# Kernel tuning notes

Measured on AMD Instinct MI355X. Metric: run time of the kernel, lower is better.

## Reference

```python
import jax, jax.numpy as jnp
import numpy as np

B, N, D = 8, 2048, 128
NEG = -9.0e15


def setup_inputs() -> dict:
    key = jax.random.key(0)
    ks = jax.random.split(key, 7)
    x = jax.random.normal(ks[0], (B, N, D), dtype=jnp.float32)
    # sparse-ish binary adjacency with self loops, stored dense as float
    adj = (jax.random.uniform(ks[1], (B, N, N)) < 0.1).astype(jnp.float32)
    adj = jnp.maximum(adj, jnp.eye(N, dtype=jnp.float32)[None])
    s = 1.0 / np.sqrt(D)
    W_w = jax.random.uniform(ks[2], (D, D), minval=-s, maxval=s, dtype=jnp.float32)
    W_b = jax.random.uniform(ks[3], (D,), minval=-s, maxval=s, dtype=jnp.float32)
    A = jnp.zeros((D, D), dtype=jnp.float32) + 0.01 * jax.random.normal(ks[4], (D, D), dtype=jnp.float32)
    s2 = 1.0 / np.sqrt(2 * D)
    gate_w = jax.random.uniform(ks[5], (1, 2 * D), minval=-s2, maxval=s2, dtype=jnp.float32)
    gate_b = jax.random.uniform(ks[6], (1,), minval=-s2, maxval=s2, dtype=jnp.float32)
    return {"x": x, "adj": adj, "W_w": W_w, "W_b": W_b, "A": A,
            "gate_w": gate_w, "gate_b": gate_b}


def reference(x, adj, W_w, W_b, A, gate_w, gate_b):
    # h = W(x): [B,N,D]
    h = jnp.einsum('bnf,df->bnd', x, W_w) + W_b
    # e[b,j,k] = (h A)[b,j,:] . h[b,k,:], then symmetrize
    hA = jnp.einsum('bnd,de->bne', h, A)
    e = jnp.einsum('bjl,bkl->bjk', hA, h)
    e = e + jnp.swapaxes(e, 1, 2)
    att = jnp.where(adj > 0, e, jnp.full_like(e, NEG))
    # NOTE: torch code softmaxes over dim=1 (the j axis)
    att = jax.nn.softmax(att, axis=1)
    att = att * adj
    h_prime = jax.nn.relu(jnp.einsum('bij,bjk->bik', att, h))
    gate_in = jnp.concatenate([x, h_prime], axis=-1)  # [B,N,2D]
    coeff = jax.nn.sigmoid(jnp.einsum('bnc,oc->bno', gate_in, gate_w) + gate_b)  # [B,N,1]
    return coeff * x + (1.0 - coeff) * h_prime
```

## Files before the change

### kernel.cpp

```cpp
#include <hip/hip_runtime.h>


#define B_ 8
#define N_ 2048
#define D_ 128

typedef __attribute__((ext_vector_type(8))) short short8;
typedef __attribute__((ext_vector_type(4))) float f32x4;

#define GLL(gp, lp) __builtin_amdgcn_global_load_lds( \
    (__attribute__((address_space(1))) const unsigned int*)(gp), \
    (__attribute__((address_space(3))) unsigned int*)(lp), 16, 0, 0)

static __device__ __forceinline__ unsigned short f2bf(float f) {
  union { float f; unsigned int u; } v; v.f = f;
  unsigned int r = v.u + 0x7fffu + ((v.u >> 16) & 1u);
  return (unsigned short)(r >> 16);
}
static __device__ __forceinline__ float bf2f(unsigned short u) {
  union { unsigned int u; float f; } v; v.u = ((unsigned int)u) << 16;
  return v.f;
}

#define CAT_OFF  ((size_t)0)
#define VT_OFF   ((size_t)8388608)
#define PUN_OFF  ((size_t)12582912)
#define S_OFF    ((size_t)79691776)
#define WB_OFF   ((size_t)79757312)
#define AT_OFF   ((size_t)79790080)
#define BITS_OFF ((size_t)79822848)

__global__ void k_cvt(const float* __restrict__ W, const float* __restrict__ A,
                      unsigned short* __restrict__ Wb1, unsigned short* __restrict__ Abt) {
  int t = threadIdx.x;
  for (int i = t; i < 128 * 128; i += 256) {
    Wb1[i] = f2bf(W[i]);
    Abt[(i & 127) * 128 + (i >> 7)] = f2bf(A[i]);
  }
}

__global__ __launch_bounds__(256) void k_bits2(const float* __restrict__ adj,
                                               unsigned int* __restrict__ bits) {
  size_t tid = (size_t)blockIdx.x * 256 + threadIdx.x;
  const float* p = adj + tid * 32;
  unsigned int m = 0;
#pragma unroll
  for (int i = 0; i < 8; i++) {
    f32x4 v = *(const f32x4*)(p + i * 4);
    m |= (v[0] > 0.f ? 1u : 0u) << (i * 4 + 0);
    m |= (v[1] > 0.f ? 1u : 0u) << (i * 4 + 1);
    m |= (v[2] > 0.f ? 1u : 0u) << (i * 4 + 2);
    m |= (v[3] > 0.f ? 1u : 0u) << (i * 4 + 3);
  }
  bits[tid] = m;
}

__global__ __launch_bounds__(256) void k1(const float* __restrict__ x,
                                          const unsigned short* __restrict__ Wb1,
                                          const float* __restrict__ Wbias,
                                          const unsigned short* __restrict__ Abt,
                                          unsigned short* __restrict__ cat) {
  __shared__ unsigned short hsm[4][16][136];
  __shared__ unsigned short hasm[4][16][136];
  const int t = threadIdx.x, w = t >> 6, lane = t & 63;
  const int q = lane >> 4, l15 = lane & 15;
  const size_t r0 = (size_t)blockIdx.x * 64 + w * 16;

  f32x4 acc[8];
#pragma unroll
  for (int dg = 0; dg < 8; dg++) acc[dg] = (f32x4){0.f, 0.f, 0.f, 0.f};
#pragma unroll
  for (int k = 0; k < 4; k++) {
    const float* xp = x + (r0 + l15) * 128 + k * 32 + q * 8;
    f32x4 xa = *(const f32x4*)xp;
    f32x4 xb = *(const f32x4*)(xp + 4);
    short8 af;
#pragma unroll
    for (int e = 0; e < 4; e++) { af[e] = (short)f2bf(xa[e]); af[4 + e] = (short)f2bf(xb[e]); }
#pragma unroll
    for (int dg = 0; dg < 8; dg++) {
      short8 bf = *(const short8*)(Wb1 + (dg * 16 + l15) * 128 + k * 32 + q * 8);
      acc[dg] = __builtin_amdgcn_mfma_f32_16x16x32_bf16(af, bf, acc[dg], 0, 0, 0);
    }
  }
#pragma unroll
  for (int dg = 0; dg < 8; dg++) {
    float bias = Wbias[dg * 16 + l15];
#pragma unroll
    for (int r = 0; r < 4; r++)
      hsm[w][q * 4 + r][dg * 16 + l15] = f2bf(acc[dg][r] + bias);
  }
  __syncthreads();
  f32x4 acc2[8];
#pragma unroll
  for (int dg = 0; dg < 8; dg++) acc2[dg] = (f32x4){0.f, 0.f, 0.f, 0.f};
#pragma unroll
  for (int k = 0; k < 4; k++) {
    short8 af = *(short8*)&hsm[w][l15][k * 32 + q * 8];
#pragma unroll
    for (int dg = 0; dg < 8; dg++) {
      short8 bf = *(const short8*)(Abt + (dg * 16 + l15) * 128 + k * 32 + q * 8);
      acc2[dg] = __builtin_amdgcn_mfma_f32_16x16x32_bf16(af, bf, acc2[dg], 0, 0, 0);
    }
  }
#pragma unroll
  for (int dg = 0; dg < 8; dg++)
#pragma unroll
    for (int r = 0; r < 4; r++)
      hasm[w][q * 4 + r][dg * 16 + l15] = f2bf(acc2[dg][r]);
  __syncthreads();
#pragma unroll
  for (int it = 0; it < 8; it++) {
    int idx = it * 64 + lane;
    int row = idx >> 5, c = idx & 31;
    short8 v = (c < 16) ? *(short8*)&hasm[w][row][c * 8]
                        : *(short8*)&hsm[w][row][(c - 16) * 8];
    *(short8*)(cat + ((r0 + row) << 8) + c * 8) = v;
  }
}

__global__ __launch_bounds__(256, 3) void k2(const unsigned short* __restrict__ cat,
                                             const unsigned int* __restrict__ bits,
                                             unsigned short* __restrict__ pun,
                                             float* __restrict__ s_out) {
  __shared__ unsigned short cj[64 * 256];
  const int t = threadIdx.x, w = t >> 6, lane = t & 63;
  const int q = lane >> 4, l15 = lane & 15;
  const int b = blockIdx.z;
  const int kbase = blockIdx.x * 128;
  const int j0b = blockIdx.y * 128;
  const size_t bN = (size_t)b * N_;
  const unsigned short* catp = cat + (bN << 8);
  const int kc = kbase + w * 32;
  const int kw = kc >> 5;
  short8 brg[2][8];
#pragma unroll
  for (int p = 0; p < 2; p++) {
    int krow = kc + 2 * l15 + p;
#pragma unroll
    for (int m = 0; m < 8; m++)
      brg[p][m] = *(const short8*)(catp + (((size_t)krow) << 8) +
                                   ((((m * 4 + q) + 16) & 31) * 8));
  }
  float acc0 = 0.f, acc1 = 0.f;
  for (int jt = 0; jt < 2; jt++) {
    const int j0 = j0b + jt * 64;
#pragma unroll
    for (int it = 0; it < 8; it++) {
      int sI = it * 256 + t;
      int row = sI >> 5, c = sI & 31;
      GLL(catp + (((size_t)(j0 + row)) << 8) + (c ^ (row & 7)) * 8,
          (char*)cj + sI * 16);
    }
    __syncthreads();
#pragma unroll
    for (int jsub = 0; jsub < 4; jsub++) {
      const int row = jsub * 16 + l15;
      short8 afr[8];
#pragma unroll
      for (int m = 0; m < 8; m++)
        afr[m] = *(short8*)(cj + row * 256 + (((m * 4 + q) ^ (l15 & 7)) * 8));
      f32x4 e0 = {0.f, 0.f, 0.f, 0.f}, e1 = {0.f, 0.f, 0.f, 0.f};
#pragma unroll
      for (int m = 0; m < 8; m++) {
        e0 = __builtin_amdgcn_mfma_f32_16x16x32_bf16(afr[m], brg[0][m], e0, 0, 0, 0);
        e1 = __builtin_amdgcn_mfma_f32_16x16x32_bf16(afr[m], brg[1][m], e1, 0, 0, 0);
      }
#pragma unroll
      for (int r = 0; r < 4; r++) {
        int jrow = j0 + jsub * 16 + q * 4 + r;
        unsigned int mb = bits[(bN + jrow) * 64 + kw];
        float x0 = ((mb >> (2 * l15)) & 1u) ? __expf(fminf(e0[r], 60.f)) : 0.f;
        float x1 = ((mb >> (2 * l15 + 1)) & 1u) ? __expf(fminf(e1[r], 60.f)) : 0.f;
        acc0 += x0; acc1 += x1;
        unsigned int pk = (unsigned int)f2bf(x0) | ((unsigned int)f2bf(x1) << 16);
        *(unsigned int*)(pun + ((bN + jrow) << 11) + kc + 2 * l15) = pk;
      }
    }
    __syncthreads();
  }
  acc0 += __shfl_xor(acc0, 16, 64); acc0 += __shfl_xor(acc0, 32, 64);
  acc1 += __shfl_xor(acc1, 16, 64); acc1 += __shfl_xor(acc1, 32, 64);
  if (lane < 16) {
    atomicAdd(&s_out[bN + kc + 2 * lane], acc0);
    atomicAdd(&s_out[bN + kc + 2 * lane + 1], acc1);
  }
}

__global__ __launch_bounds__(256) void k1v(const unsigned short* __restrict__ cat,
                                           const float* __restrict__ s,
                                           unsigned short* __restrict__ vt) {
  __shared__ unsigned short tile[64][136];
  __shared__ float rsv[64];
  const int t = threadIdx.x;
  const int b = blockIdx.y;
  const int nbase = blockIdx.x * 64;
  if (t < 64) rsv[t] = 1.f / s[(size_t)b * N_ + nbase + t];
#pragma unroll
  for (int k = 0; k < 4; k++) {
    int sI = t + 256 * k;
    int row = sI >> 4, part = sI & 15;
    *(short8*)&tile[row][part * 8] =
        *(const short8*)(cat + (((size_t)(b * N_ + nbase + row)) << 8) + 128 + part * 8);
  }
  __syncthreads();
#pragma unroll
  for (int k = 0; k < 4; k++) {
    int sI = t + 256 * k;
    int dd = sI >> 3, part = sI & 7;
    unsigned short tmp[8];
#pragma unroll
    for (int j = 0; j < 8; j++) {
      int jj = part * 8 + j;
      tmp[j] = f2bf(bf2f(tile[jj][dd]) * rsv[jj]);
    }
    *(short8*)(vt + (((size_t)(b * 128 + dd)) << 11) + nbase + part * 8) = *(short8*)tmp;
  }
}

__global__ __launch_bounds__(256) void k3(const unsigned short* __restrict__ pun,
                                          const unsigned short* __restrict__ vt,
                                          const float* __restrict__ x,
                                          const float* __restrict__ gw,
                                          const float* __restrict__ gb,
                                          float* __restrict__ out) {
  __shared__ char smem[40960];
  const int t = threadIdx.x, w = t >> 6, lane = t & 63;
  const int q = lane >> 4, l15 = lane & 15;
  const int b = blockIdx.y, i0 = blockIdx.x * 32;
  const size_t bN = (size_t)b * N_;
  unsigned short* pa = (unsigned short*)smem;
  unsigned short* vb = (unsigned short*)(smem + 8192);

  f32x4 acc[2][2];
#pragma unroll
  for (int ih = 0; ih < 2; ih++)
#pragma unroll
    for (int dh = 0; dh < 2; dh++) acc[ih][dh] = (f32x4){0.f, 0.f, 0.f, 0.f};

  for (int jt = 0; jt < N_ / 128; jt++) {
    const int j0 = jt * 128;
#pragma unroll
    for (int it = 0; it < 10; it++) {
      int sI = it * 256 + t;
      const unsigned short* g;
      if (sI < 512) {
        int row = sI >> 4, c = sI & 15;
        g = pun + (((size_t)(bN + i0 + row)) << 11) + j0 + ((c ^ (row & 7)) * 8);
      } else {
        int s2 = sI - 512;
        int dd = s2 >> 4, c = s2 & 15;
        g = vt + (((size_t)(b * 128 + dd)) << 11) + j0 + ((c ^ (dd & 7)) * 8);
      }
      GLL(g, smem + sI * 16);
    }
    __syncthreads();
#pragma unroll
    for (int ks = 0; ks < 4; ks++) {
      short8 af[2], bf[2];
#pragma unroll
      for (int ih = 0; ih < 2; ih++) {
        int m = ih * 16 + l15;
        af[ih] = *(short8*)(pa + m * 128 + (((ks * 4 + q) ^ (m & 7)) * 8));
      }
#pragma unroll
      for (int dh = 0; dh < 2; dh++) {
        int d = w * 32 + dh * 16 + l15;
        bf[dh] = *(short8*)(vb + d * 128 + (((ks * 4 + q) ^ (d & 7)) * 8));
      }
      acc[0][0] = __builtin_amdgcn_mfma_f32_16x16x32_bf16(af[0], bf[0], acc[0][0], 0, 0, 0);
      acc[0][1] = __builtin_amdgcn_mfma_f32_16x16x32_bf16(af[0], bf[1], acc[0][1], 0, 0, 0);
      acc[1][0] = __builtin_amdgcn_mfma_f32_16x16x32_bf16(af[1], bf[0], acc[1][0], 0, 0, 0);
      acc[1][1] = __builtin_amdgcn_mfma_f32_16x16x32_bf16(af[1], bf[1], acc[1][1], 0, 0, 0);
    }
    __syncthreads();
  }
  float* hs = (float*)smem;
  float* co = (float*)(smem + 16896);
#pragma unroll
  for (int ih = 0; ih < 2; ih++)
#pragma unroll
    for (int dh = 0; dh < 2; dh++)
#pragma unroll
      for (int r = 0; r < 4; r++) {
        int row = ih * 16 + q * 4 + r;
        int d = w * 32 + dh * 16 + l15;
        hs[row * 132 + d] = fmaxf(acc[ih][dh][r], 0.f);
      }
  __syncthreads();
  {
    int grow = t >> 3, sub = t & 7;
    const float* xr = x + (((size_t)(bN + i0 + grow)) << 7);
    float z = 0.f;
#pragma unroll
    for (int k = 0; k < 16; k++) {
      int dd = sub + 8 * k;
      z += gw[dd] * xr[dd] + gw[128 + dd] * hs[grow * 132 + dd];
    }
    z += __shfl_xor(z, 1, 64);
    z += __shfl_xor(z, 2, 64);
    z += __shfl_xor(z, 4, 64);
    if (sub == 0) co[grow] = 1.f / (1.f + __expf(-(z + gb[0])));
  }
  __syncthreads();
#pragma unroll
  for (int kk = 0; kk < 4; kk++) {
    int id = kk * 256 + t;
    int row = id >> 5, c4 = id & 31;
    size_t g = (((size_t)(bN + i0 + row)) << 7) + c4 * 4;
    f32x4 xv = *(const f32x4*)(x + g);
    f32x4 hv = *(const f32x4*)(hs + row * 132 + c4 * 4);
    float cf = co[row];
    f32x4 o;
#pragma unroll
    for (int e = 0; e < 4; e++) o[e] = cf * xv[e] + (1.f - cf) * hv[e];
    *(f32x4*)(out + g) = o;
  }
}

extern "C" void kernel_launch(void* const* d_in, const int* in_sizes, int n_in,
                              void* d_out, int out_size, void* d_ws, size_t ws_size,
                              hipStream_t stream) {
  const float* x   = (const float*)d_in[0];
  const float* adj = (const float*)d_in[1];
  const float* Ww  = (const float*)d_in[2];
  const float* Wb  = (const float*)d_in[3];
  const float* A   = (const float*)d_in[4];
  const float* gw  = (const float*)d_in[5];
  const float* gb  = (const float*)d_in[6];
  float* out = (float*)d_out;
  char* ws = (char*)d_ws;

  unsigned short* cat = (unsigned short*)(ws + CAT_OFF);
  unsigned short* vt  = (unsigned short*)(ws + VT_OFF);
  unsigned short* pun = (unsigned short*)(ws + PUN_OFF);
  float* s  = (float*)(ws + S_OFF);
  unsigned short* Wb1 = (unsigned short*)(ws + WB_OFF);
  unsigned short* Abt = (unsigned short*)(ws + AT_OFF);
  unsigned int* bits  = (unsigned int*)(ws + BITS_OFF);

  hipMemsetAsync(s, 0, (size_t)B_ * N_ * sizeof(float), stream);
  k_cvt<<<1, 256, 0, stream>>>(Ww, A, Wb1, Abt);
  k_bits2<<<(B_ * N_ * N_) / (256 * 32), 256, 0, stream>>>(adj, bits);
  k1<<<(B_ * N_) / 64, 256, 0, stream>>>(x, Wb1, Wb, Abt, cat);
  k2<<<dim3(N_ / 128, 16, B_), 256, 0, stream>>>(cat, bits, pun, s);
  k1v<<<dim3(N_ / 64, B_), 256, 0, stream>>>(cat, s, vt);
  k3<<<dim3(N_ / 32, B_), 256, 0, stream>>>(pun, vt, x, gw, gb, out);
}
```

Baseline: 309.0 us.

## Split k3 reduction over j into four partials and add gating epilogue kernel

Measured after the change: 350.7 us. 1.13x slower.

```diff
diff --git a/kernel.cpp b/kernel.cpp
--- a/kernel.cpp
+++ b/kernel.cpp
@@ -29,6 +29,8 @@
 #define WB_OFF   ((size_t)79757312)
 #define AT_OFF   ((size_t)79790080)
 #define BITS_OFF ((size_t)79822848)
+#define PART_OFF ((size_t)84017152)
+#define PART_SZ  ((size_t)8388608)
 
 __global__ void k_cvt(const float* __restrict__ W, const float* __restrict__ A,
                       unsigned short* __restrict__ Wb1, unsigned short* __restrict__ Abt) {
@@ -119,7 +121,7 @@
   }
 }
 
-__global__ __launch_bounds__(256, 3) void k2(const unsigned short* __restrict__ cat,
+__global__ __launch_bounds__(256, 4) void k2(const unsigned short* __restrict__ cat,
                                              const unsigned int* __restrict__ bits,
                                              unsigned short* __restrict__ pun,
                                              float* __restrict__ s_out) {
@@ -128,7 +130,7 @@
   const int q = lane >> 4, l15 = lane & 15;
   const int b = blockIdx.z;
   const int kbase = blockIdx.x * 128;
-  const int j0b = blockIdx.y * 128;
+  const int j0b = blockIdx.y * 256;
   const size_t bN = (size_t)b * N_;
   const unsigned short* catp = cat + (bN << 8);
   const int kc = kbase + w * 32;
@@ -143,7 +145,7 @@
                                    ((((m * 4 + q) + 16) & 31) * 8));
   }
   float acc0 = 0.f, acc1 = 0.f;
-  for (int jt = 0; jt < 2; jt++) {
+  for (int jt = 0; jt < 4; jt++) {
     const int j0 = j0b + jt * 64;
 #pragma unroll
     for (int it = 0; it < 8; it++) {
@@ -220,14 +222,12 @@
 
 __global__ __launch_bounds__(256) void k3(const unsigned short* __restrict__ pun,
                                           const unsigned short* __restrict__ vt,
-                                          const float* __restrict__ x,
-                                          const float* __restrict__ gw,
-                                          const float* __restrict__ gb,
-                                          float* __restrict__ out) {
+                                          float* __restrict__ out,
+                                          float* __restrict__ parts) {
   __shared__ char smem[40960];
   const int t = threadIdx.x, w = t >> 6, lane = t & 63;
   const int q = lane >> 4, l15 = lane & 15;
-  const int b = blockIdx.y, i0 = blockIdx.x * 32;
+  const int b = blockIdx.z, i0 = blockIdx.x * 32, p = blockIdx.y;
   const size_t bN = (size_t)b * N_;
   unsigned short* pa = (unsigned short*)smem;
   unsigned short* vb = (unsigned short*)(smem + 8192);
@@ -238,8 +238,8 @@
 #pragma unroll
     for (int dh = 0; dh < 2; dh++) acc[ih][dh] = (f32x4){0.f, 0.f, 0.f, 0.f};
 
-  for (int jt = 0; jt < N_ / 128; jt++) {
-    const int j0 = jt * 128;
+  for (int jt = 0; jt < 4; jt++) {
+    const int j0 = p * 512 + jt * 128;
 #pragma unroll
     for (int it = 0; it < 10; it++) {
       int sI = it * 256 + t;
@@ -276,46 +276,53 @@
     __syncthreads();
   }
   float* hs = (float*)smem;
-  float* co = (float*)(smem + 16896);
 #pragma unroll
   for (int ih = 0; ih < 2; ih++)
 #pragma unroll
     for (int dh = 0; dh < 2; dh++)
 #pragma unroll
-      for (int r = 0; r < 4; r++) {
-        int row = ih * 16 + q * 4 + r;
-        int d = w * 32 + dh * 16 + l15;
-        hs[row * 132 + d] = fmaxf(acc[ih][dh][r], 0.f);
-      }
+      for (int r = 0; r < 4; r++)
+        hs[(ih * 16 + q * 4 + r) * 132 + w * 32 + dh * 16 + l15] = acc[ih][dh][r];
   __syncthreads();
-  {
-    int grow = t >> 3, sub = t & 7;
-    const float* xr = x + (((size_t)(bN + i0 + grow)) << 7);
-    float z = 0.f;
-#pragma unroll
-    for (int k = 0; k < 16; k++) {
-      int dd = sub + 8 * k;
-      z += gw[dd] * xr[dd] + gw[128 + dd] * hs[grow * 132 + dd];
-    }
-    z += __shfl_xor(z, 1, 64);
-    z += __shfl_xor(z, 2, 64);
-    z += __shfl_xor(z, 4, 64);
-    if (sub == 0) co[grow] = 1.f / (1.f + __expf(-(z + gb[0])));
-  }
-  __syncthreads();
+  float* dst = (p == 0) ? out : (parts + (size_t)(p - 1) * (PART_SZ / 4));
 #pragma unroll
   for (int kk = 0; kk < 4; kk++) {
     int id = kk * 256 + t;
     int row = id >> 5, c4 = id & 31;
-    size_t g = (((size_t)(bN + i0 + row)) << 7) + c4 * 4;
-    f32x4 xv = *(const f32x4*)(x + g);
-    f32x4 hv = *(const f32x4*)(hs + row * 132 + c4 * 4);
-    float cf = co[row];
-    f32x4 o;
-#pragma unroll
-    for (int e = 0; e < 4; e++) o[e] = cf * xv[e] + (1.f - cf) * hv[e];
-    *(f32x4*)(out + g) = o;
-  }
+    *(f32x4*)(dst + (((size_t)(bN + i0 + row)) << 7) + c4 * 4) =
+        *(f32x4*)(hs + row * 132 + c4 * 4);
+  }
+}
+
+__global__ __launch_bounds__(256) void k4(const float* __restrict__ x,
+                                          const float* __restrict__ gw,
+                                          const float* __restrict__ gb,
+                                          float* __restrict__ out,
+                                          const float* __restrict__ parts) {
+  const int t = threadIdx.x, w = t >> 6, lane = t & 63;
+  const size_t row = (size_t)blockIdx.x * 4 + w;
+  const size_t base = (row << 7) + lane * 2;
+  float2 xv = *(const float2*)(x + base);
+  float2 hv = *(const float2*)(out + base);
+#pragma unroll
+  for (int p = 1; p < 4; p++) {
+    float2 pv = *(const float2*)(parts + (size_t)(p - 1) * (PART_SZ / 4) + base);
+    hv.x += pv.x; hv.y += pv.y;
+  }
+  hv.x = fmaxf(hv.x, 0.f); hv.y = fmaxf(hv.y, 0.f);
+  const int d = lane * 2;
+  float z = gw[d] * xv.x + gw[d + 1] * xv.y + gw[128 + d] * hv.x + gw[129 + d] * hv.y;
+  z += __shfl_xor(z, 1, 64);
+  z += __shfl_xor(z, 2, 64);
+  z += __shfl_xor(z, 4, 64);
+  z += __shfl_xor(z, 8, 64);
+  z += __shfl_xor(z, 16, 64);
+  z += __shfl_xor(z, 32, 64);
+  float c = 1.f / (1.f + __expf(-(z + gb[0])));
+  float2 o;
+  o.x = c * xv.x + (1.f - c) * hv.x;
+  o.y = c * xv.y + (1.f - c) * hv.y;
+  *(float2*)(out + base) = o;
 }
 
 extern "C" void kernel_launch(void* const* d_in, const int* in_sizes, int n_in,
@@ -338,12 +345,14 @@
   unsigned short* Wb1 = (unsigned short*)(ws + WB_OFF);
   unsigned short* Abt = (unsigned short*)(ws + AT_OFF);
   unsigned int* bits  = (unsigned int*)(ws + BITS_OFF);
+  float* parts = (float*)(ws + PART_OFF);
 
   hipMemsetAsync(s, 0, (size_t)B_ * N_ * sizeof(float), stream);
   k_cvt<<<1, 256, 0, stream>>>(Ww, A, Wb1, Abt);
   k_bits2<<<(B_ * N_ * N_) / (256 * 32), 256, 0, stream>>>(adj, bits);
   k1<<<(B_ * N_) / 64, 256, 0, stream>>>(x, Wb1, Wb, Abt, cat);
-  k2<<<dim3(N_ / 128, 16, B_), 256, 0, stream>>>(cat, bits, pun, s);
+  k2<<<dim3(N_ / 128, 8, B_), 256, 0, stream>>>(cat, bits, pun, s);
   k1v<<<dim3(N_ / 64, B_), 256, 0, stream>>>(cat, s, vt);
-  k3<<<dim3(N_ / 32, B_), 256, 0, stream>>>(pun, vt, x, gw, gb, out);
-}
+  k3<<<dim3(N_ / 32, 4, B_), 256, 0, stream>>>(pun, vt, out, parts);
+  k4<<<B_ * N_ / 4, 256, 0, stream>>>(x, gw, gb, out, parts);
+}
```
